# Performance work log

Hardware: AMD Instinct MI355X
Metric: run time of the kernel (lower is better)

Reference implementation:

```python
import jax, jax.numpy as jnp
import numpy as np

B, D, H, W = 32, 64, 32, 32
M = 1024  # codebook_size


def setup_inputs() -> dict:
    key = jax.random.key(0)
    k1, k2, k3 = jax.random.split(key, 3)
    z = jax.random.normal(k1, (B, D, H, W), dtype=jnp.float32)
    codebook = jax.random.normal(k2, (M, D), dtype=jnp.float32)
    noise = jax.random.normal(k3, (B * H * W, D), dtype=jnp.float32)
    return {"z": z, "codebook": codebook, "noise": noise}


def reference(z, codebook, noise):
    b, d, h, w = z.shape
    n = b * h * w
    # (B,D,H,W) -> (B,H,W,D) -> (N,D)
    zf = jnp.transpose(z, (0, 2, 3, 1)).reshape(n, d)
    x2 = jnp.sum(zf * zf, axis=1, keepdims=True)          # (N,1)
    y2 = jnp.sum(codebook * codebook, axis=1)[None, :]    # (1,M)
    dist = x2 + y2 - 2.0 * (zf @ codebook.T)              # (N,M)
    dist_min = jnp.min(dist, axis=1, keepdims=True)       # (N,1)
    ind = jnp.argmin(dist, axis=1)                        # (N,) int
    # noise substitution: unit-norm random direction scaled by sqrt(min dist)
    nrm = jnp.maximum(jnp.linalg.norm(noise, axis=-1, keepdims=True), 1e-9)
    q_error = noise / nrm * jnp.sqrt(jnp.maximum(dist_min, 0.0))
    z_q = zf + q_error                                    # (N,D)
    # torch: z_q.view(B, D, H*W) is a raw memory reshape of the (B*H*W, D) buffer
    z_q_view = z_q.reshape(b, d, h * w)                   # (B,D,HW)
    # loss = mean over (B,HW,HW) of z_q_view^T @ z_q_view
    #      = sum_b sum_d (sum_n z_q_view[b,d,n])^2 / (B * HW^2)  (no HWxHW intermediate)
    s = jnp.sum(z_q_view, axis=2)                         # (B,D)
    hw = h * w
    loss = jnp.sum(s * s) / (b * hw * hw)
    z_q_out = jnp.transpose(z_q.reshape(b, h, w, d), (0, 3, 1, 2))  # (B,D,H,W)
    return z_q_out, loss, ind
```

## Files before the change

### kernel.cpp

```cpp
#include <hip/hip_runtime.h>
#include <hip/hip_bf16.h>

#define BB 32
#define DD 64
#define HW 1024
#define NN 32768
#define MM 1024

typedef _Float16 half8 __attribute__((ext_vector_type(8)));
typedef float    floatx4 __attribute__((ext_vector_type(4)));

#define MFMA16(a, b, c) __builtin_amdgcn_mfma_f32_16x16x32_f16((a), (b), (c), 0, 0, 0)

#define LO_SCALE   2048.0f
#define LO_INV     (1.0f / 2048.0f)

__global__ void k_norms(const float* __restrict__ cb,
                        float* __restrict__ y2,
                        float* __restrict__ loss_slot) {
    int m = blockIdx.x * blockDim.x + threadIdx.x;
    if (m == 0) *loss_slot = 0.0f;
    if (m < MM) {
        const float4* c4 = (const float4*)(cb + (size_t)m * DD);
        float s = 0.f;
#pragma unroll
        for (int k = 0; k < 16; ++k) {
            float4 v = c4[k];
            s += v.x * v.x + v.y * v.y + v.z * v.z + v.w * v.w;
        }
        y2[m] = s;
    }
}

__global__ void k_cbprep(const float* __restrict__ cb,
                         _Float16* __restrict__ ch,
                         _Float16* __restrict__ cl) {
    int u = blockIdx.x * blockDim.x + threadIdx.x;
    if (u >= 64 * 2 * 64) return;
    int lane  = u & 63;
    int kstep = (u >> 6) & 1;
    int mtile = u >> 7;
    int m  = mtile * 16 + (lane & 15);
    int d0 = kstep * 32 + ((lane >> 4) & 3) * 8;
    const float* src = cb + (size_t)m * DD + d0;
    half8 h, l;
#pragma unroll
    for (int j = 0; j < 8; ++j) {
        float x = -2.0f * src[j];
        _Float16 hi = (_Float16)x;
        _Float16 lo = (_Float16)((x - (float)hi) * LO_SCALE);
        h[j] = hi;
        l[j] = lo;
    }
    *(half8*)(ch + (size_t)u * 8) = h;
    *(half8*)(cl + (size_t)u * 8) = l;
}

__global__ __launch_bounds__(256, 2) void k_dist(const float* __restrict__ z,
                                                 const _Float16* __restrict__ ch,
                                                 const _Float16* __restrict__ cl,
                                                 const float* __restrict__ y2,
                                                 float* __restrict__ dmin_out,
                                                 float* __restrict__ ind_out) {
    __shared__ float zt[64][65];
    __shared__ float y2s[MM];
    __shared__ float x2p[64][4];
    __shared__ float x2s[64];
    __shared__ float bestv_s[4][64];
    __shared__ int   besti_s[4][64];

    const int t    = threadIdx.x;
    const int lane = t & 63;
    const int wv   = t >> 6;
    const int quad = lane >> 4;
    const int col  = lane & 15;
    const int blk  = blockIdx.x;
    const int b    = blk >> 4;
    const int hw0  = (blk & 15) << 6;

    const float* zbase = z + ((size_t)b << 16) + hw0;

    for (int i = t; i < 64 * 64; i += 256) {
        int d = i >> 6, r = i & 63;
        zt[r][d] = zbase[(size_t)d * HW + r];
    }
    for (int i = t; i < MM; i += 256) y2s[i] = y2[i];
    __syncthreads();

    {
        int row = t & 63, seg = t >> 6;
        float s = 0.f;
#pragma unroll
        for (int j = 0; j < 16; ++j) {
            float v = zt[row][seg * 16 + j];
            s = __builtin_fmaf(v, v, s);
        }
        x2p[row][seg] = s;
    }

    half8 ah[4][2], al[4][2];
#pragma unroll
    for (int nt = 0; nt < 4; ++nt) {
        int row = nt * 16 + col;
#pragma unroll
        for (int ks = 0; ks < 2; ++ks) {
            int d0 = ks * 32 + quad * 8;
            half8 h, l;
#pragma unroll
            for (int j = 0; j < 8; ++j) {
                float x = zt[row][d0 + j];
                _Float16 hi = (_Float16)x;
                _Float16 lo = (_Float16)((x - (float)hi) * LO_SCALE);
                h[j] = hi;
                l[j] = lo;
            }
            ah[nt][ks] = h;
            al[nt][ks] = l;
        }
    }
    __syncthreads();
    if (t < 64) x2s[t] = x2p[t][0] + x2p[t][1] + x2p[t][2] + x2p[t][3];

    const half8* ch8 = (const half8*)ch;
    const half8* cl8 = (const half8*)cl;

    float best[16];
    int   bmt[16];
#pragma unroll
    for (int s = 0; s < 16; ++s) { best[s] = 1e30f; bmt[s] = 0; }

    const int mt0 = wv * 16;
    half8 bh0 = ch8[((mt0 * 2 + 0) << 6) + lane];
    half8 bl0 = cl8[((mt0 * 2 + 0) << 6) + lane];
    half8 bh1 = ch8[((mt0 * 2 + 1) << 6) + lane];
    half8 bl1 = cl8[((mt0 * 2 + 1) << 6) + lane];

#pragma unroll 2
    for (int i = 0; i < 16; ++i) {
        const int mt  = mt0 + i;
        const int mtn = mt + (i < 15 ? 1 : 0);
        half8 nh0 = ch8[((mtn * 2 + 0) << 6) + lane];
        half8 nl0 = cl8[((mtn * 2 + 0) << 6) + lane];
        half8 nh1 = ch8[((mtn * 2 + 1) << 6) + lane];
        half8 nl1 = cl8[((mtn * 2 + 1) << 6) + lane];

        float y2v = y2s[(mt << 4) + col];
        floatx4 a1[4], a2[4];
#pragma unroll
        for (int nt = 0; nt < 4; ++nt) {
            floatx4 i1 = {y2v, y2v, y2v, y2v};
            floatx4 i2 = {0.f, 0.f, 0.f, 0.f};
            a1[nt] = i1;
            a2[nt] = i2;
        }
#pragma unroll
        for (int nt = 0; nt < 4; ++nt) {
            a1[nt] = MFMA16(ah[nt][0], bh0, a1[nt]);
            a2[nt] = MFMA16(al[nt][0], bh0, a2[nt]);
            a2[nt] = MFMA16(ah[nt][0], bl0, a2[nt]);
            a1[nt] = MFMA16(ah[nt][1], bh1, a1[nt]);
            a2[nt] = MFMA16(al[nt][1], bh1, a2[nt]);
            a2[nt] = MFMA16(ah[nt][1], bl1, a2[nt]);
        }
#pragma unroll
        for (int nt = 0; nt < 4; ++nt) {
#pragma unroll
            for (int r = 0; r < 4; ++r) {
                float v = __builtin_fmaf(a2[nt][r], LO_INV, a1[nt][r]);
                int s = nt * 4 + r;
                bool c = v < best[s];
                best[s] = c ? v : best[s];
                bmt[s]  = c ? mt : bmt[s];
            }
        }
        bh0 = nh0; bl0 = nl0; bh1 = nh1; bl1 = nl1;
    }

#pragma unroll
    for (int nt = 0; nt < 4; ++nt) {
#pragma unroll
        for (int r = 0; r < 4; ++r) {
            int s = nt * 4 + r;
            float v  = best[s];
            int  idx = bmt[s] * 16 + col;
#pragma unroll
            for (int mask = 1; mask <= 8; mask <<= 1) {
                float v2 = __shfl_xor(v, mask);
                int   i2 = __shfl_xor(idx, mask);
                if (v2 < v || (v2 == v && i2 < idx)) { v = v2; idx = i2; }
            }
            if (col == 0) {
                int rl = nt * 16 + quad * 4 + r;
                bestv_s[wv][rl] = v;
                besti_s[wv][rl] = idx;
            }
        }
    }
    __syncthreads();

    if (t < 64) {
        float bv = bestv_s[0][t];
        int   bi = besti_s[0][t];
#pragma unroll
        for (int w = 1; w < 4; ++w) {
            float v = bestv_s[w][t];
            int   ix = besti_s[w][t];
            if (v < bv || (v == bv && ix < bi)) { bv = v; bi = ix; }
        }
        int n = (blk << 6) + t;
        dmin_out[n] = x2s[t] + bv;
        ind_out[n]  = (float)bi;
    }
}

__global__ __launch_bounds__(256) void k_out(const float* __restrict__ z,
                                             const float* __restrict__ noise,
                                             const float* __restrict__ dmin,
                                             float* __restrict__ zq,
                                             float* __restrict__ loss_slot) {
    __shared__ float nt[64][65];
    __shared__ float snorm[64];
    __shared__ float scale[64];
    __shared__ float partials[256];
    __shared__ float sq[4];

    const int t   = threadIdx.x;
    const int blk = blockIdx.x;
    const int b   = blk >> 4;
    const int hw0 = (blk & 15) << 6;
    const int n0  = (blk << 6);

    const float4* noise4 = (const float4*)noise;
    const size_t base4 = (size_t)blk * 1024;
#pragma unroll
    for (int k = 0; k < 4; ++k) {
        int v = t + 256 * k;
        float4 vv = noise4[base4 + v];
        int c  = v >> 4;
        int d0 = (v & 15) << 2;
        nt[d0 + 0][c] = vv.x;
        nt[d0 + 1][c] = vv.y;
        nt[d0 + 2][c] = vv.z;
        nt[d0 + 3][c] = vv.w;
        float p = vv.x * vv.x + vv.y * vv.y + vv.z * vv.z + vv.w * vv.w;
        p += __shfl_xor(p, 1);
        p += __shfl_xor(p, 2);
        p += __shfl_xor(p, 4);
        p += __shfl_xor(p, 8);
        if ((t & 15) == 0) snorm[c] = p;
    }
    __syncthreads();

    if (t < 64) {
        float dm = dmin[n0 + t];
        float nr = sqrtf(snorm[t]);
        nr = fmaxf(nr, 1e-9f);
        scale[t] = sqrtf(fmaxf(dm, 0.f)) / nr;
    }
    __syncthreads();

    float acc = 0.f;
    const size_t obase = ((size_t)b << 16) + hw0;
#pragma unroll
    for (int it = 0; it < 16; ++it) {
        int flat = it * 256 + t;
        int d = flat >> 6;
        int c = t & 63;
        size_t idx = obase + (size_t)d * HW + c;
        float v = z[idx] + nt[d][c] * scale[c];
        zq[idx] = v;
        acc += v;
    }

    partials[t] = acc;
    __syncthreads();
    if (t < 4) {
        float s = 0.f;
        for (int w = 0; w < 4; ++w)
            for (int j = 0; j < 16; ++j)
                s += partials[w * 64 + t * 16 + j];
        sq[t] = s * s;
    }
    __syncthreads();
    if (t == 0) {
        float contrib = (sq[0] + sq[1] + sq[2] + sq[3]) * (1.0f / 33554432.0f);
        atomicAdd(loss_slot, contrib);
    }
}

extern "C" void kernel_launch(void* const* d_in, const int* in_sizes, int n_in,
                              void* d_out, int out_size, void* d_ws, size_t ws_size,
                              hipStream_t stream) {
    const float* z        = (const float*)d_in[0];
    const float* codebook = (const float*)d_in[1];
    const float* noise    = (const float*)d_in[2];

    float* out      = (float*)d_out;
    float* zq_out   = out;
    float* loss_ptr = out + 2097152;
    float* ind_out  = out + 2097153;

    float* y2       = (float*)d_ws;
    float* dmin     = y2 + MM;
    _Float16* ch    = (_Float16*)(dmin + NN);
    _Float16* cl    = ch + 65536;

    k_norms <<<4,  256, 0, stream>>>(codebook, y2, loss_ptr);
    k_cbprep<<<32, 256, 0, stream>>>(codebook, ch, cl);
    k_dist  <<<512, 256, 0, stream>>>(z, ch, cl, y2, dmin, ind_out);
    k_out   <<<512, 256, 0, stream>>>(z, noise, dmin, zq_out, loss_ptr);
}
```

Baseline: 107.5 us.

## Fuse distance and output kernels, merge codebook prep, widen blocks to 512 threads

Merges the two codebook preprocessing kernels into one and fuses the distance/argmin kernel with the noise-substitution output kernel, so z is read once from LDS rather than re-read from global memory and dmin no longer goes through a workspace round trip. Blocks grow to 512 threads (8 waves). Each wave covers half the rows and a quarter of the codebook, halving per-wave accumulator registers. This removes two launches and the global traffic for dmin and the second z read, at the cost of more LDS per block (noise tile staged alongside z) and possibly lower occupancy.

New measurement: 98.72 us. -8.2%, faster.

```diff
diff --git a/kernel.cpp b/kernel.cpp
--- a/kernel.cpp
+++ b/kernel.cpp
@@ -15,63 +15,70 @@
 #define LO_SCALE   2048.0f
 #define LO_INV     (1.0f / 2048.0f)
 
-__global__ void k_norms(const float* __restrict__ cb,
-                        float* __restrict__ y2,
-                        float* __restrict__ loss_slot) {
-    int m = blockIdx.x * blockDim.x + threadIdx.x;
-    if (m == 0) *loss_slot = 0.0f;
-    if (m < MM) {
-        const float4* c4 = (const float4*)(cb + (size_t)m * DD);
+__global__ void k_prep(const float* __restrict__ cb,
+                       _Float16* __restrict__ ch,
+                       _Float16* __restrict__ cl,
+                       float* __restrict__ y2,
+                       float* __restrict__ loss_slot) {
+    int u = blockIdx.x * blockDim.x + threadIdx.x;
+    if (u == 0) *loss_slot = 0.0f;
+
+    if (u < 64 * 2 * 64) {
+        int lane  = u & 63;
+        int kstep = (u >> 6) & 1;
+        int mtile = u >> 7;
+        int m  = mtile * 16 + (lane & 15);
+        int d0 = kstep * 32 + ((lane >> 4) & 3) * 8;
+        const float* src = cb + (size_t)m * DD + d0;
+        half8 h, l;
+#pragma unroll
+        for (int j = 0; j < 8; ++j) {
+            float x = -2.0f * src[j];
+            _Float16 hi = (_Float16)x;
+            _Float16 lo = (_Float16)((x - (float)hi) * LO_SCALE);
+            h[j] = hi;
+            l[j] = lo;
+        }
+        *(half8*)(ch + (size_t)u * 8) = h;
+        *(half8*)(cl + (size_t)u * 8) = l;
+    }
+
+    if (u < MM) {
+        const float4* c4 = (const float4*)(cb + (size_t)u * DD);
         float s = 0.f;
 #pragma unroll
         for (int k = 0; k < 16; ++k) {
             float4 v = c4[k];
             s += v.x * v.x + v.y * v.y + v.z * v.z + v.w * v.w;
         }
-        y2[m] = s;
+        y2[u] = s;
     }
 }
 
-__global__ void k_cbprep(const float* __restrict__ cb,
-                         _Float16* __restrict__ ch,
-                         _Float16* __restrict__ cl) {
-    int u = blockIdx.x * blockDim.x + threadIdx.x;
-    if (u >= 64 * 2 * 64) return;
-    int lane  = u & 63;
-    int kstep = (u >> 6) & 1;
-    int mtile = u >> 7;
-    int m  = mtile * 16 + (lane & 15);
-    int d0 = kstep * 32 + ((lane >> 4) & 3) * 8;
-    const float* src = cb + (size_t)m * DD + d0;
-    half8 h, l;
-#pragma unroll
-    for (int j = 0; j < 8; ++j) {
-        float x = -2.0f * src[j];
-        _Float16 hi = (_Float16)x;
-        _Float16 lo = (_Float16)((x - (float)hi) * LO_SCALE);
-        h[j] = hi;
-        l[j] = lo;
-    }
-    *(half8*)(ch + (size_t)u * 8) = h;
-    *(half8*)(cl + (size_t)u * 8) = l;
-}
-
-__global__ __launch_bounds__(256, 2) void k_dist(const float* __restrict__ z,
+__global__ __launch_bounds__(512, 4) void k_main(const float* __restrict__ z,
+                                                 const float* __restrict__ noise,
                                                  const _Float16* __restrict__ ch,
                                                  const _Float16* __restrict__ cl,
                                                  const float* __restrict__ y2,
-                                                 float* __restrict__ dmin_out,
-                                                 float* __restrict__ ind_out) {
+                                                 float* __restrict__ zq,
+                                                 float* __restrict__ ind_out,
+                                                 float* __restrict__ loss_slot) {
     __shared__ float zt[64][65];
+    __shared__ float nt[64][65];
     __shared__ float y2s[MM];
-    __shared__ float x2p[64][4];
-    __shared__ float x2s[64];
+    __shared__ float x2p[64][8];
+    __shared__ float snorm[64];
+    __shared__ float scale_s[64];
     __shared__ float bestv_s[4][64];
     __shared__ int   besti_s[4][64];
+    __shared__ float partials[512];
+    __shared__ float sq[4];
 
     const int t    = threadIdx.x;
     const int lane = t & 63;
     const int wv   = t >> 6;
+    const int nth  = wv & 1;
+    const int cq   = wv >> 1;
     const int quad = lane >> 4;
     const int col  = lane & 15;
     const int blk  = blockIdx.x;
@@ -80,28 +87,50 @@
 
     const float* zbase = z + ((size_t)b << 16) + hw0;
 
-    for (int i = t; i < 64 * 64; i += 256) {
+    for (int i = t; i < 64 * 64; i += 512) {
         int d = i >> 6, r = i & 63;
         zt[r][d] = zbase[(size_t)d * HW + r];
     }
-    for (int i = t; i < MM; i += 256) y2s[i] = y2[i];
+    for (int i = t; i < MM; i += 512) y2s[i] = y2[i];
+
+    {
+        const float4* noise4 = (const float4*)noise;
+        const size_t base4 = (size_t)blk * 1024;
+#pragma unroll
+        for (int k = 0; k < 2; ++k) {
+            int v = t + 512 * k;
+            float4 vv = noise4[base4 + v];
+            int c  = v >> 4;
+            int d0 = (v & 15) << 2;
+            nt[d0 + 0][c] = vv.x;
+            nt[d0 + 1][c] = vv.y;
+            nt[d0 + 2][c] = vv.z;
+            nt[d0 + 3][c] = vv.w;
+            float p = vv.x * vv.x + vv.y * vv.y + vv.z * vv.z + vv.w * vv.w;
+            p += __shfl_xor(p, 1);
+            p += __shfl_xor(p, 2);
+            p += __shfl_xor(p, 4);
+            p += __shfl_xor(p, 8);
+            if ((t & 15) == 0) snorm[c] = p;
+        }
+    }
     __syncthreads();
 
     {
         int row = t & 63, seg = t >> 6;
         float s = 0.f;
 #pragma unroll
-        for (int j = 0; j < 16; ++j) {
-            float v = zt[row][seg * 16 + j];
+        for (int j = 0; j < 8; ++j) {
+            float v = zt[row][seg * 8 + j];
             s = __builtin_fmaf(v, v, s);
         }
         x2p[row][seg] = s;
     }
 
-    half8 ah[4][2], al[4][2];
-#pragma unroll
-    for (int nt = 0; nt < 4; ++nt) {
-        int row = nt * 16 + col;
+    half8 ah[2][2], al[2][2];
+#pragma unroll
+    for (int nt2 = 0; nt2 < 2; ++nt2) {
+        int row = nth * 32 + nt2 * 16 + col;
 #pragma unroll
         for (int ks = 0; ks < 2; ++ks) {
             int d0 = ks * 32 + quad * 8;
@@ -114,22 +143,21 @@
                 h[j] = hi;
                 l[j] = lo;
             }
-            ah[nt][ks] = h;
-            al[nt][ks] = l;
-        }
-    }
-    __syncthreads();
-    if (t < 64) x2s[t] = x2p[t][0] + x2p[t][1] + x2p[t][2] + x2p[t][3];
+            ah[nt2][ks] = h;
+            al[nt2][ks] = l;
+        }
+    }
+    __syncthreads();
 
     const half8* ch8 = (const half8*)ch;
     const half8* cl8 = (const half8*)cl;
 
-    float best[16];
-    int   bmt[16];
-#pragma unroll
-    for (int s = 0; s < 16; ++s) { best[s] = 1e30f; bmt[s] = 0; }
-
-    const int mt0 = wv * 16;
+    float best[8];
+    int   bmt[8];
+#pragma unroll
+    for (int s = 0; s < 8; ++s) { best[s] = 1e30f; bmt[s] = 0; }
+
+    const int mt0 = cq * 16;
     half8 bh0 = ch8[((mt0 * 2 + 0) << 6) + lane];
     half8 bl0 = cl8[((mt0 * 2 + 0) << 6) + lane];
     half8 bh1 = ch8[((mt0 * 2 + 1) << 6) + lane];
@@ -145,29 +173,29 @@
         half8 nl1 = cl8[((mtn * 2 + 1) << 6) + lane];
 
         float y2v = y2s[(mt << 4) + col];
-        floatx4 a1[4], a2[4];
-#pragma unroll
-        for (int nt = 0; nt < 4; ++nt) {
+        floatx4 a1[2], a2[2];
+#pragma unroll
+        for (int n2 = 0; n2 < 2; ++n2) {
             floatx4 i1 = {y2v, y2v, y2v, y2v};
             floatx4 i2 = {0.f, 0.f, 0.f, 0.f};
-            a1[nt] = i1;
-            a2[nt] = i2;
-        }
-#pragma unroll
-        for (int nt = 0; nt < 4; ++nt) {
-            a1[nt] = MFMA16(ah[nt][0], bh0, a1[nt]);
-            a2[nt] = MFMA16(al[nt][0], bh0, a2[nt]);
-            a2[nt] = MFMA16(ah[nt][0], bl0, a2[nt]);
-            a1[nt] = MFMA16(ah[nt][1], bh1, a1[nt]);
-            a2[nt] = MFMA16(al[nt][1], bh1, a2[nt]);
-            a2[nt] = MFMA16(ah[nt][1], bl1, a2[nt]);
-        }
-#pragma unroll
-        for (int nt = 0; nt < 4; ++nt) {
+            a1[n2] = i1;
+            a2[n2] = i2;
+        }
+#pragma unroll
+        for (int n2 = 0; n2 < 2; ++n2) {
+            a1[n2] = MFMA16(ah[n2][0], bh0, a1[n2]);
+            a2[n2] = MFMA16(al[n2][0], bh0, a2[n2]);
+            a2[n2] = MFMA16(ah[n2][0], bl0, a2[n2]);
+            a1[n2] = MFMA16(ah[n2][1], bh1, a1[n2]);
+            a2[n2] = MFMA16(al[n2][1], bh1, a2[n2]);
+            a2[n2] = MFMA16(ah[n2][1], bl1, a2[n2]);
+        }
+#pragma unroll
+        for (int n2 = 0; n2 < 2; ++n2) {
 #pragma unroll
             for (int r = 0; r < 4; ++r) {
-                float v = __builtin_fmaf(a2[nt][r], LO_INV, a1[nt][r]);
-                int s = nt * 4 + r;
+                float v = __builtin_fmaf(a2[n2][r], LO_INV, a1[n2][r]);
+                int s = n2 * 4 + r;
                 bool c = v < best[s];
                 best[s] = c ? v : best[s];
                 bmt[s]  = c ? mt : bmt[s];
@@ -177,10 +205,10 @@
     }
 
 #pragma unroll
-    for (int nt = 0; nt < 4; ++nt) {
+    for (int n2 = 0; n2 < 2; ++n2) {
 #pragma unroll
         for (int r = 0; r < 4; ++r) {
-            int s = nt * 4 + r;
+            int s = n2 * 4 + r;
             float v  = best[s];
             int  idx = bmt[s] * 16 + col;
 #pragma unroll
@@ -190,9 +218,9 @@
                 if (v2 < v || (v2 == v && i2 < idx)) { v = v2; idx = i2; }
             }
             if (col == 0) {
-                int rl = nt * 16 + quad * 4 + r;
-                bestv_s[wv][rl] = v;
-                besti_s[wv][rl] = idx;
+                int rl = nth * 32 + n2 * 16 + quad * 4 + r;
+                bestv_s[cq][rl] = v;
+                besti_s[cq][rl] = idx;
             }
         }
     }
@@ -207,68 +235,26 @@
             int   ix = besti_s[w][t];
             if (v < bv || (v == bv && ix < bi)) { bv = v; bi = ix; }
         }
+        float x2 = 0.f;
+#pragma unroll
+        for (int s = 0; s < 8; ++s) x2 += x2p[t][s];
+        float dm = x2 + bv;
         int n = (blk << 6) + t;
-        dmin_out[n] = x2s[t] + bv;
-        ind_out[n]  = (float)bi;
-    }
-}
-
-__global__ __launch_bounds__(256) void k_out(const float* __restrict__ z,
-                                             const float* __restrict__ noise,
-                                             const float* __restrict__ dmin,
-                                             float* __restrict__ zq,
-                                             float* __restrict__ loss_slot) {
-    __shared__ float nt[64][65];
-    __shared__ float snorm[64];
-    __shared__ float scale[64];
-    __shared__ float partials[256];
-    __shared__ float sq[4];
-
-    const int t   = threadIdx.x;
-    const int blk = blockIdx.x;
-    const int b   = blk >> 4;
-    const int hw0 = (blk & 15) << 6;
-    const int n0  = (blk << 6);
-
-    const float4* noise4 = (const float4*)noise;
-    const size_t base4 = (size_t)blk * 1024;
-#pragma unroll
-    for (int k = 0; k < 4; ++k) {
-        int v = t + 256 * k;
-        float4 vv = noise4[base4 + v];
-        int c  = v >> 4;
-        int d0 = (v & 15) << 2;
-        nt[d0 + 0][c] = vv.x;
-        nt[d0 + 1][c] = vv.y;
-        nt[d0 + 2][c] = vv.z;
-        nt[d0 + 3][c] = vv.w;
-        float p = vv.x * vv.x + vv.y * vv.y + vv.z * vv.z + vv.w * vv.w;
-        p += __shfl_xor(p, 1);
-        p += __shfl_xor(p, 2);
-        p += __shfl_xor(p, 4);
-        p += __shfl_xor(p, 8);
-        if ((t & 15) == 0) snorm[c] = p;
-    }
-    __syncthreads();
-
-    if (t < 64) {
-        float dm = dmin[n0 + t];
-        float nr = sqrtf(snorm[t]);
-        nr = fmaxf(nr, 1e-9f);
-        scale[t] = sqrtf(fmaxf(dm, 0.f)) / nr;
+        ind_out[n] = (float)bi;
+        float nr = fmaxf(sqrtf(snorm[t]), 1e-9f);
+        scale_s[t] = sqrtf(fmaxf(dm, 0.f)) / nr;
     }
     __syncthreads();
 
     float acc = 0.f;
     const size_t obase = ((size_t)b << 16) + hw0;
 #pragma unroll
-    for (int it = 0; it < 16; ++it) {
-        int flat = it * 256 + t;
+    for (int it = 0; it < 8; ++it) {
+        int flat = it * 512 + t;
         int d = flat >> 6;
         int c = t & 63;
-        size_t idx = obase + (size_t)d * HW + c;
-        float v = z[idx] + nt[d][c] * scale[c];
-        zq[idx] = v;
+        float v = zt[c][d] + nt[d][c] * scale_s[c];
+        zq[obase + (size_t)d * HW + c] = v;
         acc += v;
     }
 
@@ -276,9 +262,9 @@
     __syncthreads();
     if (t < 4) {
         float s = 0.f;
-        for (int w = 0; w < 4; ++w)
+        for (int g = 0; g < 8; ++g)
             for (int j = 0; j < 16; ++j)
-                s += partials[w * 64 + t * 16 + j];
+                s += partials[g * 64 + t * 16 + j];
         sq[t] = s * s;
     }
     __syncthreads();
@@ -301,12 +287,10 @@
     float* ind_out  = out + 2097153;
 
     float* y2       = (float*)d_ws;
-    float* dmin     = y2 + MM;
-    _Float16* ch    = (_Float16*)(dmin + NN);
+    _Float16* ch    = (_Float16*)(y2 + MM);
     _Float16* cl    = ch + 65536;
 
-    k_norms <<<4,  256, 0, stream>>>(codebook, y2, loss_ptr);
-    k_cbprep<<<32, 256, 0, stream>>>(codebook, ch, cl);
-    k_dist  <<<512, 256, 0, stream>>>(z, ch, cl, y2, dmin, ind_out);
-    k_out   <<<512, 256, 0, stream>>>(z, noise, dmin, zq_out, loss_ptr);
+    k_prep<<<16,  512, 0, stream>>>(codebook, ch, cl, y2, loss_ptr);
+    k_main<<<512, 512, 0, stream>>>(z, noise, ch, cl, y2,
+                                    zq_out, ind_out, loss_ptr);
 }
```
